# Optimization experiments

Hardware: AMD Instinct MI355X
Metric: run time of the kernel (lower is better)

Reference implementation:

```python
import jax, jax.numpy as jnp
import numpy as np

B, S, H = 32768, 16, 16  # batch, seq_len, G_hiddensize (code requires H == S and H == latent_dim == 16)
LATENT = 16
DISC_DIMS = [(1, 32), (32, 16), (16, 8), (8, 16), (16, 32)]


def setup_inputs() -> dict:
    key = jax.random.key(0)
    ks = iter(jax.random.split(key, 64))
    def p(shape, scale=0.1):
        return (jax.random.normal(next(ks), shape, dtype=jnp.float32) * scale)
    inp = dict(
        values=jax.random.normal(next(ks), (B, S), dtype=jnp.float32),
        masks=jax.random.randint(next(ks), (B, S), 0, 2).astype(jnp.int32),
        g_fwd_Wih=p((4 * H, 1)), g_fwd_Whh=p((4 * H, H)), g_fwd_b=p((4 * H,)),
        g_bwd_Wih=p((4 * H, 1)), g_bwd_Whh=p((4 * H, H)), g_bwd_b=p((4 * H,)),
        imp_W=p((1, H)), imp_b=p((1,)),
        fc_W=p((LATENT, H)), fc_b=p((LATENT,)),
        dec_Wih=p((4 * H, LATENT)), dec_Whh=p((4 * H, H)), dec_b=p((4 * H,)),
        dec_out_W=p((1, H)), dec_out_b=p((1,)),
        disc_out_W=p((1, 32)), disc_out_b=p((1,)),
    )
    for k, (i, h) in enumerate(DISC_DIMS):
        inp[f"d_W_{k}"] = p((4 * h, i))
        inp[f"d_b_{k}"] = p((4 * h,))
    return inp


def lstm_cell(x, h, c, Wih, Whh, b):
    gates = x @ Wih.T + h @ Whh.T + b
    i, f, g, o = jnp.split(gates, 4, axis=-1)
    c = jax.nn.sigmoid(f) * c + jax.nn.sigmoid(i) * jnp.tanh(g)
    h = jax.nn.sigmoid(o) * jnp.tanh(c)
    return h, c


def _forward(values, masks, g_fwd_Wih, g_fwd_Whh, g_fwd_b, g_bwd_Wih, g_bwd_Whh, g_bwd_b,
             imp_W, imp_b, fc_W, fc_b, dec_Wih, dec_Whh, dec_b, dec_out_W, dec_out_b,
             disc_out_W, disc_out_b,
             d_W_0, d_b_0, d_W_1, d_b_1, d_W_2, d_b_2, d_W_3, d_b_3, d_W_4, d_b_4):
    dt = values.dtype
    Bsz = values.shape[0]
    x = values[:, :, None]                     # (B, S, 1)
    m = masks.astype(dt)[:, :, None]           # (B, S, 1)
    # NOTE: torch.flip along axis 2 (size 1) is a no-op, so the bwd cell sees the
    # same (un-reversed) sequence as the fwd cell -- faithfully reproduced here.
    zH = jnp.zeros((Bsz, H), dt)
    h_f, c_f = lstm_cell(jnp.full((Bsz, 1), 128.0, dt), zH, zH, g_fwd_Wih, g_fwd_Whh, g_fwd_b)
    h_b, c_b = lstm_cell(jnp.full((Bsz, 1), -128.0, dt), zH, zH, g_bwd_Wih, g_bwd_Whh, g_bwd_b)

    def gen_step(carry, xm):
        h_f, c_f, h_b, c_b = carry
        x_t, m_t = xm                          # (B,1) each
        cc_f = (1 - m_t) * x_t + m_t * (h_f @ imp_W.T + imp_b)
        cc_b = (1 - m_t) * x_t + m_t * (h_b @ imp_W.T + imp_b)
        h_f, c_f = lstm_cell(cc_f, h_f, c_f, g_fwd_Wih, g_fwd_Whh, g_fwd_b)
        h_b, c_b = lstm_cell(cc_b, h_b, c_b, g_bwd_Wih, g_bwd_Whh, g_bwd_b)
        return (h_f, c_f, h_b, c_b), None

    (h_f, c_f, h_b, c_b), _ = jax.lax.scan(
        gen_step, (h_f, c_f, h_b, c_b),
        (jnp.transpose(x, (1, 0, 2)), jnp.transpose(m, (1, 0, 2))))
    h = h_f + h_b                               # (B, H), H == S
    imputations = h.reshape(Bsz, S, 1)
    imputed = imputations * (1 - m) + x * m      # (B, S, 1)

    # Discriminator: torch calls each LSTMCell WITHOUT state every timestep, so
    # hidden/cell start at zero each call -> purely feedforward per (batch, t).
    # W_hh @ 0 == 0, so only W_ih and the combined bias matter. Vectorize over B*S.
    inp = imputed.reshape(Bsz * S, 1)
    for W, b in ((d_W_0, d_b_0), (d_W_1, d_b_1), (d_W_2, d_b_2), (d_W_3, d_b_3), (d_W_4, d_b_4)):
        gates = inp @ W.T + b
        i, f, g, o = jnp.split(gates, 4, axis=-1)
        cc = jax.nn.sigmoid(i) * jnp.tanh(g)
        inp = jax.nn.sigmoid(o) * jnp.tanh(cc)
    disc_output = (inp @ disc_out_W.T + disc_out_b).reshape(Bsz, S, 1)

    latent = h @ fc_W.T + fc_b                  # (B, 16)

    # Decoder: ignores latent values (only uses batch size); start token = 128s.
    hd = cd = jnp.zeros((Bsz, H), dt)
    hd, cd = lstm_cell(jnp.full((Bsz, LATENT), 128.0, dt), hd, cd, dec_Wih, dec_Whh, dec_b)

    def dec_step(carry, _):
        hd, cd = carry
        hd, cd = lstm_cell(cd, hd, cd, dec_Wih, dec_Whh, dec_b)
        return (hd, cd), hd @ dec_out_W.T + dec_out_b

    _, outs = jax.lax.scan(dec_step, (hd, cd), None, length=S)  # (S, B, 1)
    reconstructed = jnp.transpose(outs, (1, 0, 2))
    return imputed, disc_output, latent, reconstructed


def reference(values, masks, g_fwd_Wih, g_fwd_Whh, g_fwd_b, g_bwd_Wih, g_bwd_Whh, g_bwd_b,
              imp_W, imp_b, fc_W, fc_b, dec_Wih, dec_Whh, dec_b, dec_out_W, dec_out_b,
              disc_out_W, disc_out_b,
              d_W_0, d_b_0, d_W_1, d_b_1, d_W_2, d_b_2, d_W_3, d_b_3, d_W_4, d_b_4):
    return _forward(values, masks, g_fwd_Wih, g_fwd_Whh, g_fwd_b, g_bwd_Wih, g_bwd_Whh, g_bwd_b,
                    imp_W, imp_b, fc_W, fc_b, dec_Wih, dec_Whh, dec_b, dec_out_W, dec_out_b,
                    disc_out_W, disc_out_b,
                    d_W_0, d_b_0, d_W_1, d_b_1, d_W_2, d_b_2, d_W_3, d_b_3, d_W_4, d_b_4)
```

## Files before the change

### kernel.cpp

```cpp
#include <hip/hip_runtime.h>

#define BB 32768
#define BS (BB*16)

typedef __attribute__((ext_vector_type(8))) short bf8v;
typedef __attribute__((ext_vector_type(4))) float f4v;

#define RECO 64
#define TAB  128
#define NTAB 2049
#define HFO  8448
#define HBO  (HFO+BS)

#define PW0 0
#define PB0 96
#define PW1 192
#define PB1 1920
#define PW2 1968
#define PB2 2448
#define PW3 2472
#define PB3 3048
#define PW4 3096
#define PB4 5016
#define POW 5112
#define POB 5144
#define PNU 5148

#define WVF 848
#define SMF 3392

#define NSCAN 1024
#define NTABB 129
#define DECB  (NSCAN + NTABB)

__device__ __forceinline__ float sigm(float x){
    return __builtin_amdgcn_rcpf(1.f + __expf(-x));
}
__device__ __forceinline__ float tanh_f(float x){
    return 1.f - 2.f * __builtin_amdgcn_rcpf(1.f + __expf(2.f * x));
}
__device__ __forceinline__ float dunit(float gi, float gg, float go){
    return sigm(go) * tanh_f(sigm(gi) * tanh_f(gg));
}
__device__ __forceinline__ unsigned short f2bf(float f){
    union { float f; unsigned int i; } v; v.f = f;
    unsigned int x = v.i;
    unsigned int r = x + 0x7fffu + ((x >> 16) & 1u);
    return (unsigned short)(r >> 16);
}
__device__ __forceinline__ float bfu(unsigned short s){
    union { unsigned u; float f; } v; v.u = ((unsigned)s) << 16; return v.f;
}
__device__ __forceinline__ float bflo(unsigned p){
    union { unsigned u; float f; } v; v.u = p << 16; return v.f;
}
__device__ __forceinline__ float bfhi(unsigned p){
    union { unsigned u; float f; } v; v.u = p & 0xffff0000u; return v.f;
}

struct P29 { const float* p[29]; };

__device__ __forceinline__ bf8v makeB(const float* Whh, const float* Wih,
                                      int row, int quad)
{
    bf8v B = {0,0,0,0,0,0,0,0};
    if (quad < 2) {
        const float4* p = (const float4*)(Whh + row*16 + quad*8);
        float4 a0 = p[0], a1 = p[1];
        B[0]=(short)f2bf(a0.x); B[1]=(short)f2bf(a0.y);
        B[2]=(short)f2bf(a0.z); B[3]=(short)f2bf(a0.w);
        B[4]=(short)f2bf(a1.x); B[5]=(short)f2bf(a1.y);
        B[6]=(short)f2bf(a1.z); B[7]=(short)f2bf(a1.w);
    } else if (quad == 2) {
        B[0] = (short)f2bf(Wih[row]);
    }
    return B;
}

__global__ __launch_bounds__(256)
void k_main(P29 a, const int* __restrict__ masks, float* __restrict__ ws)
{
    __shared__ __align__(16) float smem[SMF];
    int tid = threadIdx.x;

    if (blockIdx.x < NSCAN) {
        int lane = tid & 63;
        int wv   = tid >> 6;
        int n    = lane & 15;
        int quad = lane >> 4;
        int dir  = (int)(blockIdx.x >= 512);
        int gid0 = blockIdx.x * 64 + wv * 16;
        int b0   = gid0 & 32767;
        float* wbase = smem + wv * WVF;
        float* xs    = wbase;
        int*   msI   = (int*)(wbase + 320);
        unsigned short* hbp = (unsigned short*)(wbase + 640);
        float* ccf   = wbase + 832;
        const int4* hbI = (const int4*)hbp;
        {
            size_t gbase = (size_t)b0 * 16;
            int e = lane * 4;
            float4 xv = *(const float4*)(a.p[0] + gbase + e);
            int4   mv = *(const int4*)(masks + gbase + e);
            int sm = lane >> 2;
            int st = (lane & 3) * 4;
            xs[(st+0)*20 + sm] = xv.x;  msI[(st+0)*20 + sm] = mv.x;
            xs[(st+1)*20 + sm] = xv.y;  msI[(st+1)*20 + sm] = mv.y;
            xs[(st+2)*20 + sm] = xv.z;  msI[(st+2)*20 + sm] = mv.z;
            xs[(st+3)*20 + sm] = xv.w;  msI[(st+3)*20 + sm] = mv.w;
        }
        const float* __restrict__ Wih = a.p[2 + 3*dir];
        const float* __restrict__ Whh = a.p[3 + 3*dir];
        const float* __restrict__ bia = a.p[4 + 3*dir];
        bf8v Bi = makeB(Whh, Wih, n,      quad);
        bf8v Bf = makeB(Whh, Wih, 16+n,   quad);
        bf8v Bg = makeB(Whh, Wih, 32+n,   quad);
        bf8v Bo = makeB(Whh, Wih, 48+n,   quad);
        bf8v Bp = {0,0,0,0,0,0,0,0};
        if (quad < 2) {
            const float4* p = (const float4*)(a.p[8] + quad*8);
            float4 a0 = p[0], a1 = p[1];
            Bp[0]=(short)f2bf(a0.x); Bp[1]=(short)f2bf(a0.y);
            Bp[2]=(short)f2bf(a0.z); Bp[3]=(short)f2bf(a0.w);
            Bp[4]=(short)f2bf(a1.x); Bp[5]=(short)f2bf(a1.y);
            Bp[6]=(short)f2bf(a1.z); Bp[7]=(short)f2bf(a1.w);
        }
        float impb = a.p[9][0];
        float bi_ = bia[n], bf_ = bia[16+n], bg_ = bia[32+n], bo_ = bia[48+n];
        float sgn = dir ? -128.f : 128.f;
        float c0, h0;
        {
            float gi0 = sgn*Wih[n]    + bi_;
            float gg0 = sgn*Wih[32+n] + bg_;
            float go0 = sgn*Wih[48+n] + bo_;
            c0 = sigm(gi0) * tanh_f(gg0);
            h0 = sigm(go0) * tanh_f(c0);
        }
        float c[4] = {c0, c0, c0, c0};
        float h[4];
        {
            unsigned short hb0 = f2bf(h0);
            #pragma unroll
            for (int r = 0; r < 4; r++) hbp[(quad*4+r)*24 + n] = hb0;
        }
        const f4v cz = {0.f, 0.f, 0.f, 0.f};
        const bf8v Az = {0,0,0,0,0,0,0,0};
        for (int t = 0; t < 16; t++) {
            union { int4 i4; bf8v b; } au;
            au.i4 = hbI[n*3 + (quad & 1)];
            bf8v A = (quad < 2) ? au.b : Az;
            f4v dimp = __builtin_amdgcn_mfma_f32_16x16x32_bf16(A, Bp, cz, 0, 0, 0);
            float4 xt4 = *(const float4*)(xs + t*20 + quad*4);
            int4   mt4 = *(const int4*)(msI + t*20 + quad*4);
            float cc0 = mt4.x ? (dimp[0] + impb) : xt4.x;
            float cc1 = mt4.y ? (dimp[1] + impb) : xt4.y;
            float cc2 = mt4.z ? (dimp[2] + impb) : xt4.z;
            float cc3 = mt4.w ? (dimp[3] + impb) : xt4.w;
            if (n == 0) {
                ccf[quad*4+0] = cc0; ccf[quad*4+1] = cc1;
                ccf[quad*4+2] = cc2; ccf[quad*4+3] = cc3;
            }
            if (quad == 2) A[0] = (short)f2bf(ccf[n]);
            f4v di = __builtin_amdgcn_mfma_f32_16x16x32_bf16(A, Bi, cz, 0, 0, 0);
            f4v df = __builtin_amdgcn_mfma_f32_16x16x32_bf16(A, Bf, cz, 0, 0, 0);
            f4v dg = __builtin_amdgcn_mfma_f32_16x16x32_bf16(A, Bg, cz, 0, 0, 0);
            f4v dO = __builtin_amdgcn_mfma_f32_16x16x32_bf16(A, Bo, cz, 0, 0, 0);
            #pragma unroll
            for (int r = 0; r < 4; r++) {
                float gi = di[r] + bi_;
                float gf = df[r] + bf_;
                float gg = dg[r] + bg_;
                float go = dO[r] + bo_;
                float cn = sigm(gf)*c[r] + sigm(gi)*tanh_f(gg);
                c[r] = cn;
                float hh = sigm(go)*tanh_f(cn);
                h[r] = hh;
                hbp[(quad*4+r)*24 + n] = f2bf(hh);
            }
        }
        float* outp = ws + HFO + (size_t)dir*BS + (size_t)b0*16;
        #pragma unroll
        for (int r = 0; r < 4; r++) outp[(quad*4+r)*16 + n] = h[r];
        return;
    }

    if (blockIdx.x < DECB) {
        unsigned short* wl = (unsigned short*)smem;
#define STAGE(WS, BSi, h, K, padK, wdst, bdst) \
    { const float* Wp = a.p[WS]; const float* Bp2 = a.p[BSi]; \
      for (int i = tid; i < 3*(h)*(K); i += 256){ \
        int r = i/(K), k = i - r*(K); int g = r/(h), u0 = r - g*(h); \
        int sr = (g==0? u0 : (g==1? 2*(h)+u0 : 3*(h)+u0)); \
        wl[(wdst) + r*(padK) + k] = f2bf(Wp[sr*(K) + k]); } \
      for (int i = tid; i < 3*(h); i += 256){ \
        int g = i/(h), u0 = i - g*(h); \
        int sr = (g==0? u0 : (g==1? 2*(h)+u0 : 3*(h)+u0)); \
        wl[(bdst) + i] = f2bf(Bp2[sr]); } }
        STAGE(19, 20, 32,  1,  1, PW0, PB0)
        STAGE(21, 22, 16, 32, 36, PW1, PB1)
        STAGE(23, 24,  8, 16, 20, PW2, PB2)
        STAGE(25, 26, 16,  8, 12, PW3, PB3)
        STAGE(27, 28, 32, 16, 20, PW4, PB4)
#undef STAGE
        { const float* s = a.p[17]; for (int i = tid; i < 32; i += 256) wl[POW+i] = f2bf(s[i]); }
        if (tid == 0) wl[POB] = f2bf(a.p[18][0]);
        __syncthreads();
        int u = tid & 15;
        int gbase = (tid & 63) & 48;
        int gid = (blockIdx.x - NSCAN) * 16 + (tid >> 4);
        const uint2* w2 = (const uint2*)wl;
        float xin = -8.f + (float)gid * (1.f/128.f);
        float lo = dunit(xin*bfu(wl[PW0+u])    + bfu(wl[PB0+u]),
                         xin*bfu(wl[PW0+32+u]) + bfu(wl[PB0+32+u]),
                         xin*bfu(wl[PW0+64+u]) + bfu(wl[PB0+64+u]));
        float hi = dunit(xin*bfu(wl[PW0+16+u]) + bfu(wl[PB0+16+u]),
                         xin*bfu(wl[PW0+48+u]) + bfu(wl[PB0+48+u]),
                         xin*bfu(wl[PW0+80+u]) + bfu(wl[PB0+80+u]));
        float A0[32];
        #pragma unroll
        for (int k = 0; k < 16; k++) { A0[k] = __shfl(lo, gbase+k); A0[16+k] = __shfl(hi, gbase+k); }
        float gi = bfu(wl[PB1+u]), gg = bfu(wl[PB1+16+u]), go = bfu(wl[PB1+32+u]);
        int bi_ = (PW1 + u*36)>>2, bg_ = (PW1 + (16+u)*36)>>2, bo_ = (PW1 + (32+u)*36)>>2;
        #pragma unroll
        for (int q = 0; q < 8; q++) {
            uint2 wi = w2[bi_+q], wg = w2[bg_+q], wo = w2[bo_+q];
            float b0=A0[4*q], b1=A0[4*q+1], b2=A0[4*q+2], b3=A0[4*q+3];
            gi += b0*bflo(wi.x) + b1*bfhi(wi.x) + b2*bflo(wi.y) + b3*bfhi(wi.y);
            gg += b0*bflo(wg.x) + b1*bfhi(wg.x) + b2*bflo(wg.y) + b3*bfhi(wg.y);
            go += b0*bflo(wo.x) + b1*bfhi(wo.x) + b2*bflo(wo.y) + b3*bfhi(wo.y);
        }
        float a1 = dunit(gi, gg, go);
        float A1[16];
        #pragma unroll
        for (int k = 0; k < 16; k++) A1[k] = __shfl(a1, gbase+k);
        int v = u & 7;
        gi = bfu(wl[PB2+v]); gg = bfu(wl[PB2+8+v]); go = bfu(wl[PB2+16+v]);
        bi_ = (PW2 + v*20)>>2; bg_ = (PW2 + (8+v)*20)>>2; bo_ = (PW2 + (16+v)*20)>>2;
        #pragma unroll
        for (int q = 0; q < 4; q++) {
            uint2 wi = w2[bi_+q], wg = w2[bg_+q], wo = w2[bo_+q];
            float b0=A1[4*q], b1=A1[4*q+1], b2=A1[4*q+2], b3=A1[4*q+3];
            gi += b0*bflo(wi.x) + b1*bfhi(wi.x) + b2*bflo(wi.y) + b3*bfhi(wi.y);
            gg += b0*bflo(wg.x) + b1*bfhi(wg.x) + b2*bflo(wg.y) + b3*bfhi(wg.y);
            go += b0*bflo(wo.x) + b1*bfhi(wo.x) + b2*bflo(wo.y) + b3*bfhi(wo.y);
        }
        float a2 = dunit(gi, gg, go);
        float A2[8];
        #pragma unroll
        for (int k = 0; k < 8; k++) A2[k] = __shfl(a2, gbase+k);
        gi = bfu(wl[PB3+u]); gg = bfu(wl[PB3+16+u]); go = bfu(wl[PB3+32+u]);
        bi_ = (PW3 + u*12)>>2; bg_ = (PW3 + (16+u)*12)>>2; bo_ = (PW3 + (32+u)*12)>>2;
        #pragma unroll
        for (int q = 0; q < 2; q++) {
            uint2 wi = w2[bi_+q], wg = w2[bg_+q], wo = w2[bo_+q];
            float b0=A2[4*q], b1=A2[4*q+1], b2=A2[4*q+2], b3=A2[4*q+3];
            gi += b0*bflo(wi.x) + b1*bfhi(wi.x) + b2*bflo(wi.y) + b3*bfhi(wi.y);
            gg += b0*bflo(wg.x) + b1*bfhi(wg.x) + b2*bflo(wg.y) + b3*bfhi(wg.y);
            go += b0*bflo(wo.x) + b1*bfhi(wo.x) + b2*bflo(wo.y) + b3*bfhi(wo.y);
        }
        float a3 = dunit(gi, gg, go);
        float A3[16];
        #pragma unroll
        for (int k = 0; k < 16; k++) A3[k] = __shfl(a3, gbase+k);
        float part;
        {
            float g0i = bfu(wl[PB4+u]),    g0g = bfu(wl[PB4+32+u]), g0o = bfu(wl[PB4+64+u]);
            float g1i = bfu(wl[PB4+16+u]), g1g = bfu(wl[PB4+48+u]), g1o = bfu(wl[PB4+80+u]);
            int c0i = (PW4 + u*20)>>2,      c0g = (PW4 + (32+u)*20)>>2, c0o = (PW4 + (64+u)*20)>>2;
            int c1i = (PW4 + (16+u)*20)>>2, c1g = (PW4 + (48+u)*20)>>2, c1o = (PW4 + (80+u)*20)>>2;
            #pragma unroll
            for (int q = 0; q < 4; q++) {
                float b0=A3[4*q], b1=A3[4*q+1], b2=A3[4*q+2], b3=A3[4*q+3];
                uint2 wi = w2[c0i+q], wg = w2[c0g+q], wo = w2[c0o+q];
                g0i += b0*bflo(wi.x) + b1*bfhi(wi.x) + b2*bflo(wi.y) + b3*bfhi(wi.y);
                g0g += b0*bflo(wg.x) + b1*bfhi(wg.x) + b2*bflo(wg.y) + b3*bfhi(wg.y);
                g0o += b0*bflo(wo.x) + b1*bfhi(wo.x) + b2*bflo(wo.y) + b3*bfhi(wo.y);
                wi = w2[c1i+q]; wg = w2[c1g+q]; wo = w2[c1o+q];
                g1i += b0*bflo(wi.x) + b1*bfhi(wi.x) + b2*bflo(wi.y) + b3*bfhi(wi.y);
                g1g += b0*bflo(wg.x) + b1*bfhi(wg.x) + b2*bflo(wg.y) + b3*bfhi(wg.y);
                g1o += b0*bflo(wo.x) + b1*bfhi(wo.x) + b2*bflo(wo.y) + b3*bfhi(wo.y);
            }
            part = dunit(g0i, g0g, g0o)*bfu(wl[POW+u]) + dunit(g1i, g1g, g1o)*bfu(wl[POW+16+u]);
        }
        part += __shfl_xor(part, 1);
        part += __shfl_xor(part, 2);
        part += __shfl_xor(part, 4);
        part += __shfl_xor(part, 8);
        if (u == 0 && gid < NTAB) ws[TAB + gid] = part + bfu(wl[POB]);
        return;
    }

    {
        float* dh = smem;
        float* dc = smem + 16;
        const float* Wih = a.p[12];
        const float* Whh = a.p[13];
        const float* bb  = a.p[14];
        const float* oW  = a.p[15];
        const float* ob  = a.p[16];
        float wii[16], wff[16], wgg[16], woo[16];
        float vii[16], vff[16], vgg[16], voo[16];
        float bi_r=0, bf_r=0, bg_r=0, bo_r=0;
        if (tid < 16) {
            int uu = tid;
            #pragma unroll
            for (int k = 0; k < 16; k++) {
                wii[k]=Wih[uu*16+k];      vii[k]=Whh[uu*16+k];
                wff[k]=Wih[(16+uu)*16+k]; vff[k]=Whh[(16+uu)*16+k];
                wgg[k]=Wih[(32+uu)*16+k]; vgg[k]=Whh[(32+uu)*16+k];
                woo[k]=Wih[(48+uu)*16+k]; voo[k]=Whh[(48+uu)*16+k];
            }
            bi_r=bb[uu]; bf_r=bb[16+uu]; bg_r=bb[32+uu]; bo_r=bb[48+uu];
            float gi = bi_r, gg = bg_r, go = bo_r;
            #pragma unroll
            for (int k = 0; k < 16; k++) {
                gi += 128.f * wii[k];
                gg += 128.f * wgg[k];
                go += 128.f * woo[k];
            }
            float cd0 = sigm(gi) * tanh_f(gg);
            dc[tid] = cd0; dh[tid] = sigm(go) * tanh_f(cd0);
        }
        __syncthreads();
        for (int t = 0; t < 16; t++) {
            float rx[16], rh[16], cold = 0.f;
            if (tid < 16) {
                #pragma unroll
                for (int k = 0; k < 16; k++) { rx[k] = dc[k]; rh[k] = dh[k]; }
                cold = dc[tid];
            }
            __syncthreads();
            if (tid < 16) {
                float gi = bi_r, gf = bf_r, gg = bg_r, go = bo_r;
                #pragma unroll
                for (int k = 0; k < 16; k++) {
                    gi += rx[k]*wii[k] + rh[k]*vii[k];
                    gf += rx[k]*wff[k] + rh[k]*vff[k];
                    gg += rx[k]*wgg[k] + rh[k]*vgg[k];
                    go += rx[k]*woo[k] + rh[k]*voo[k];
                }
                float cn = sigm(gf)*cold + sigm(gi)*tanh_f(gg);
                dc[tid] = cn; dh[tid] = sigm(go)*tanh_f(cn);
            }
            __syncthreads();
            if (tid == 0) {
                float o = ob[0];
                #pragma unroll
                for (int k = 0; k < 16; k++) o += dh[k] * oW[k];
                ws[RECO + t] = o;
            }
            __syncthreads();
        }
    }
}

__global__ __launch_bounds__(256) void k_post(P29 a, const int* __restrict__ masks,
                                              const float* __restrict__ ws,
                                              float* __restrict__ out)
{
    __shared__ float tab[NTAB];
    __shared__ __align__(16) float fw[256];
    __shared__ __align__(16) float rec[16];
    __shared__ float fb[16];
    int tid = threadIdx.x;
    for (int i = tid; i < NTAB; i += 256) tab[i] = ws[TAB + i];
    fw[tid] = a.p[10][tid];
    if (tid < 16) { fb[tid] = a.p[11][tid]; rec[tid] = ws[RECO + tid]; }
    __syncthreads();
    int T = blockIdx.x * 256 + tid;
    int b = T >> 2;
    int q = T & 3;
    int tq = q * 4;
    const float4* hf4 = (const float4*)(ws + HFO + (size_t)b*16);
    const float4* hb4 = (const float4*)(ws + HBO + (size_t)b*16);
    float4 s0, s1, s2, s3;
    {
        float4 f0=hf4[0], f1=hf4[1], f2=hf4[2], f3=hf4[3];
        float4 g0=hb4[0], g1=hb4[1], g2=hb4[2], g3=hb4[3];
        s0 = make_float4(f0.x+g0.x, f0.y+g0.y, f0.z+g0.z, f0.w+g0.w);
        s1 = make_float4(f1.x+g1.x, f1.y+g1.y, f1.z+g1.z, f1.w+g1.w);
        s2 = make_float4(f2.x+g2.x, f2.y+g2.y, f2.z+g2.z, f2.w+g2.w);
        s3 = make_float4(f3.x+g3.x, f3.y+g3.y, f3.z+g3.z, f3.w+g3.w);
    }
    float4 hq = (q==0) ? s0 : (q==1) ? s1 : (q==2) ? s2 : s3;
    float4 xv = *(const float4*)(a.p[0] + (size_t)b*16 + tq);
    int4   mv = *(const int4*)(masks + (size_t)b*16 + tq);
    float impv[4];
    impv[0] = mv.x ? xv.x : hq.x;
    impv[1] = mv.y ? xv.y : hq.y;
    impv[2] = mv.z ? xv.z : hq.z;
    impv[3] = mv.w ? xv.w : hq.w;
    float latv[4];
    #pragma unroll
    for (int j = 0; j < 4; j++) {
        int t = tq + j;
        const float4* wr = (const float4*)(fw + t*16);
        float4 w0=wr[0], w1=wr[1], w2=wr[2], w3=wr[3];
        float l = fb[t];
        l += s0.x*w0.x + s0.y*w0.y + s0.z*w0.z + s0.w*w0.w;
        l += s1.x*w1.x + s1.y*w1.y + s1.z*w1.z + s1.w*w1.w;
        l += s2.x*w2.x + s2.y*w2.y + s2.z*w2.z + s2.w*w2.w;
        l += s3.x*w3.x + s3.y*w3.y + s3.z*w3.z + s3.w*w3.w;
        latv[j] = l;
    }
    float dv[4];
    #pragma unroll
    for (int j = 0; j < 4; j++) {
        float xx = fminf(fmaxf(impv[j], -8.f), 8.f);
        float f = (xx + 8.f) * 128.f;
        float fi = floorf(f);
        int i = (int)fi; i = i > NTAB-2 ? NTAB-2 : i;
        float w = f - fi;
        dv[j] = fmaf(w, tab[i+1] - tab[i], tab[i]);
    }
    float4 rv = ((const float4*)rec)[q];
    size_t eo = (size_t)b*16 + tq;
    *(float4*)(out + eo)        = make_float4(impv[0], impv[1], impv[2], impv[3]);
    *(float4*)(out + BS + eo)   = make_float4(dv[0], dv[1], dv[2], dv[3]);
    *(float4*)(out + 2*BS + eo) = make_float4(latv[0], latv[1], latv[2], latv[3]);
    *(float4*)(out + 3*BS + eo) = rv;
}

extern "C" void kernel_launch(void* const* d_in, const int* in_sizes, int n_in,
                              void* d_out, int out_size, void* d_ws, size_t ws_size,
                              hipStream_t stream)
{
    float* ws = (float*)d_ws;
    P29 a;
    for (int i = 0; i < 29; i++) a.p[i] = (const float*)d_in[i];
    const int* masks = (const int*)d_in[1];
    k_main<<<NSCAN + NTABB + 1, 256, 0, stream>>>(a, masks, ws);
    k_post<<<(BB*4)/256, 256, 0, stream>>>(a, masks, ws, (float*)d_out);
}
```

Baseline: 164.2 us.

## Transpose scan MFMA operands, pass hidden state via bpermute, reorder block roles

The generator LSTM scan now treats the weights as the MFMA A operand and the hidden state as B, so each lane holds one batch row. The recurrent state moves between lanes with ds_bpermute and packed bf16 converts instead of round-tripping through shared memory. Biases are folded into the MFMA accumulator inputs, and x and mask values are read straight from global per row instead of being staged in LDS. Block order also changes so the decoder and table blocks run first, and the shared memory footprint shrinks, which may raise occupancy. In exchange the per-step lane exchange adds bpermute latency on the serial dependency chain, and the output store pattern changes.

After: 154.0 us. 1.07x faster.

```diff
diff --git a/kernel.cpp b/kernel.cpp
--- a/kernel.cpp
+++ b/kernel.cpp
@@ -26,12 +26,10 @@
 #define POB 5144
 #define PNU 5148
 
-#define WVF 848
-#define SMF 3392
+#define SMF 2580
 
 #define NSCAN 1024
 #define NTABB 129
-#define DECB  (NSCAN + NTABB)
 
 __device__ __forceinline__ float sigm(float x){
     return __builtin_amdgcn_rcpf(1.f + __expf(-x));
@@ -83,108 +81,118 @@
     __shared__ __align__(16) float smem[SMF];
     int tid = threadIdx.x;
 
-    if (blockIdx.x < NSCAN) {
+    if (blockIdx.x >= NTABB + 1) {
         int lane = tid & 63;
         int wv   = tid >> 6;
-        int n    = lane & 15;
+        int m    = lane & 15;
         int quad = lane >> 4;
-        int dir  = (int)(blockIdx.x >= 512);
-        int gid0 = blockIdx.x * 64 + wv * 16;
+        int sb   = blockIdx.x - (NTABB + 1);
+        int dir  = sb >= 512 ? 1 : 0;
+        int gid0 = sb * 64 + wv * 16;
         int b0   = gid0 & 32767;
-        float* wbase = smem + wv * WVF;
-        float* xs    = wbase;
-        int*   msI   = (int*)(wbase + 320);
-        unsigned short* hbp = (unsigned short*)(wbase + 640);
-        float* ccf   = wbase + 832;
-        const int4* hbI = (const int4*)hbp;
-        {
-            size_t gbase = (size_t)b0 * 16;
-            int e = lane * 4;
-            float4 xv = *(const float4*)(a.p[0] + gbase + e);
-            int4   mv = *(const int4*)(masks + gbase + e);
-            int sm = lane >> 2;
-            int st = (lane & 3) * 4;
-            xs[(st+0)*20 + sm] = xv.x;  msI[(st+0)*20 + sm] = mv.x;
-            xs[(st+1)*20 + sm] = xv.y;  msI[(st+1)*20 + sm] = mv.y;
-            xs[(st+2)*20 + sm] = xv.z;  msI[(st+2)*20 + sm] = mv.z;
-            xs[(st+3)*20 + sm] = xv.w;  msI[(st+3)*20 + sm] = mv.w;
-        }
+
         const float* __restrict__ Wih = a.p[2 + 3*dir];
         const float* __restrict__ Whh = a.p[3 + 3*dir];
         const float* __restrict__ bia = a.p[4 + 3*dir];
-        bf8v Bi = makeB(Whh, Wih, n,      quad);
-        bf8v Bf = makeB(Whh, Wih, 16+n,   quad);
-        bf8v Bg = makeB(Whh, Wih, 32+n,   quad);
-        bf8v Bo = makeB(Whh, Wih, 48+n,   quad);
-        bf8v Bp = {0,0,0,0,0,0,0,0};
+
+        bf8v Ai = makeB(Whh, Wih, m,      quad);
+        bf8v Af = makeB(Whh, Wih, 16+m,   quad);
+        bf8v Ag = makeB(Whh, Wih, 32+m,   quad);
+        bf8v Ao = makeB(Whh, Wih, 48+m,   quad);
+        bf8v Ap = {0,0,0,0,0,0,0,0};
         if (quad < 2) {
             const float4* p = (const float4*)(a.p[8] + quad*8);
             float4 a0 = p[0], a1 = p[1];
-            Bp[0]=(short)f2bf(a0.x); Bp[1]=(short)f2bf(a0.y);
-            Bp[2]=(short)f2bf(a0.z); Bp[3]=(short)f2bf(a0.w);
-            Bp[4]=(short)f2bf(a1.x); Bp[5]=(short)f2bf(a1.y);
-            Bp[6]=(short)f2bf(a1.z); Bp[7]=(short)f2bf(a1.w);
+            Ap[0]=(short)f2bf(a0.x); Ap[1]=(short)f2bf(a0.y);
+            Ap[2]=(short)f2bf(a0.z); Ap[3]=(short)f2bf(a0.w);
+            Ap[4]=(short)f2bf(a1.x); Ap[5]=(short)f2bf(a1.y);
+            Ap[6]=(short)f2bf(a1.z); Ap[7]=(short)f2bf(a1.w);
         }
         float impb = a.p[9][0];
-        float bi_ = bia[n], bf_ = bia[16+n], bg_ = bia[32+n], bo_ = bia[48+n];
+        f4v cimp = {impb, impb, impb, impb};
+
+        f4v cbi, cbf, cbg, cbo;
+        {
+            float4 t;
+            t = *(const float4*)(bia +      quad*4); cbi = (f4v){t.x,t.y,t.z,t.w};
+            t = *(const float4*)(bia + 16 + quad*4); cbf = (f4v){t.x,t.y,t.z,t.w};
+            t = *(const float4*)(bia + 32 + quad*4); cbg = (f4v){t.x,t.y,t.z,t.w};
+            t = *(const float4*)(bia + 48 + quad*4); cbo = (f4v){t.x,t.y,t.z,t.w};
+        }
+
         float sgn = dir ? -128.f : 128.f;
-        float c0, h0;
+        float c[4], hl[4];
         {
-            float gi0 = sgn*Wih[n]    + bi_;
-            float gg0 = sgn*Wih[32+n] + bg_;
-            float go0 = sgn*Wih[48+n] + bo_;
-            c0 = sigm(gi0) * tanh_f(gg0);
-            h0 = sigm(go0) * tanh_f(c0);
-        }
-        float c[4] = {c0, c0, c0, c0};
-        float h[4];
-        {
-            unsigned short hb0 = f2bf(h0);
-            #pragma unroll
-            for (int r = 0; r < 4; r++) hbp[(quad*4+r)*24 + n] = hb0;
-        }
-        const f4v cz = {0.f, 0.f, 0.f, 0.f};
-        const bf8v Az = {0,0,0,0,0,0,0,0};
-        for (int t = 0; t < 16; t++) {
-            union { int4 i4; bf8v b; } au;
-            au.i4 = hbI[n*3 + (quad & 1)];
-            bf8v A = (quad < 2) ? au.b : Az;
-            f4v dimp = __builtin_amdgcn_mfma_f32_16x16x32_bf16(A, Bp, cz, 0, 0, 0);
-            float4 xt4 = *(const float4*)(xs + t*20 + quad*4);
-            int4   mt4 = *(const int4*)(msI + t*20 + quad*4);
-            float cc0 = mt4.x ? (dimp[0] + impb) : xt4.x;
-            float cc1 = mt4.y ? (dimp[1] + impb) : xt4.y;
-            float cc2 = mt4.z ? (dimp[2] + impb) : xt4.z;
-            float cc3 = mt4.w ? (dimp[3] + impb) : xt4.w;
-            if (n == 0) {
-                ccf[quad*4+0] = cc0; ccf[quad*4+1] = cc1;
-                ccf[quad*4+2] = cc2; ccf[quad*4+3] = cc3;
-            }
-            if (quad == 2) A[0] = (short)f2bf(ccf[n]);
-            f4v di = __builtin_amdgcn_mfma_f32_16x16x32_bf16(A, Bi, cz, 0, 0, 0);
-            f4v df = __builtin_amdgcn_mfma_f32_16x16x32_bf16(A, Bf, cz, 0, 0, 0);
-            f4v dg = __builtin_amdgcn_mfma_f32_16x16x32_bf16(A, Bg, cz, 0, 0, 0);
-            f4v dO = __builtin_amdgcn_mfma_f32_16x16x32_bf16(A, Bo, cz, 0, 0, 0);
+            float4 wI = *(const float4*)(Wih +      quad*4);
+            float4 wG = *(const float4*)(Wih + 32 + quad*4);
+            float4 wO = *(const float4*)(Wih + 48 + quad*4);
+            float wIv[4] = {wI.x, wI.y, wI.z, wI.w};
+            float wGv[4] = {wG.x, wG.y, wG.z, wG.w};
+            float wOv[4] = {wO.x, wO.y, wO.z, wO.w};
             #pragma unroll
             for (int r = 0; r < 4; r++) {
-                float gi = di[r] + bi_;
-                float gf = df[r] + bf_;
-                float gg = dg[r] + bg_;
-                float go = dO[r] + bo_;
-                float cn = sigm(gf)*c[r] + sigm(gi)*tanh_f(gg);
-                c[r] = cn;
-                float hh = sigm(go)*tanh_f(cn);
-                h[r] = hh;
-                hbp[(quad*4+r)*24 + n] = f2bf(hh);
+                float gi0 = sgn*wIv[r] + cbi[r];
+                float gg0 = sgn*wGv[r] + cbg[r];
+                float go0 = sgn*wOv[r] + cbo[r];
+                float c0 = sigm(gi0) * tanh_f(gg0);
+                c[r] = c0;
+                hl[r] = sigm(go0) * tanh_f(c0);
+            }
+        }
+        unsigned u01, u23;
+        asm("v_cvt_pk_bf16_f32 %0, %1, %2" : "=v"(u01) : "v"(hl[0]), "v"(hl[1]));
+        asm("v_cvt_pk_bf16_f32 %0, %1, %2" : "=v"(u23) : "v"(hl[2]), "v"(hl[3]));
+
+        int pa0 = ((m + quad*32)      & 63) << 2;
+        int pa1 = ((m + quad*32 + 16) & 63) << 2;
+
+        const float* xrow = a.p[0] + (size_t)(b0 + m) * 16;
+        const int*   mrow = masks  + (size_t)(b0 + m) * 16;
+
+        #pragma unroll
+        for (int t4 = 0; t4 < 4; t4++) {
+            float4 x4 = *(const float4*)(xrow + t4*4);
+            int4   m4 = *(const int4*)(mrow + t4*4);
+            float xa[4] = {x4.x, x4.y, x4.z, x4.w};
+            int   ma[4] = {m4.x, m4.y, m4.z, m4.w};
+            #pragma unroll
+            for (int j = 0; j < 4; j++) {
+                union { int i[4]; bf8v v; } B;
+                int w0 = __builtin_amdgcn_ds_bpermute(pa0, (int)u01);
+                int w1 = __builtin_amdgcn_ds_bpermute(pa0, (int)u23);
+                int w2 = __builtin_amdgcn_ds_bpermute(pa1, (int)u01);
+                int w3 = __builtin_amdgcn_ds_bpermute(pa1, (int)u23);
+                bool hi2 = quad >= 2;
+                B.i[0] = hi2 ? 0 : w0;
+                B.i[1] = hi2 ? 0 : w1;
+                B.i[2] = hi2 ? 0 : w2;
+                B.i[3] = hi2 ? 0 : w3;
+                f4v dimp = __builtin_amdgcn_mfma_f32_16x16x32_bf16(Ap, B.v, cimp, 0, 0, 0);
+                float cc = ma[j] ? dimp[0] : xa[j];
+                unsigned ccw;
+                asm("v_cvt_pk_bf16_f32 %0, %1, %2" : "=v"(ccw) : "v"(cc), "v"(0.f));
+                B.i[0] = (quad == 2) ? (int)ccw : B.i[0];
+                f4v di  = __builtin_amdgcn_mfma_f32_16x16x32_bf16(Ai, B.v, cbi, 0, 0, 0);
+                f4v df_ = __builtin_amdgcn_mfma_f32_16x16x32_bf16(Af, B.v, cbf, 0, 0, 0);
+                f4v dg  = __builtin_amdgcn_mfma_f32_16x16x32_bf16(Ag, B.v, cbg, 0, 0, 0);
+                f4v dO  = __builtin_amdgcn_mfma_f32_16x16x32_bf16(Ao, B.v, cbo, 0, 0, 0);
+                #pragma unroll
+                for (int r = 0; r < 4; r++) {
+                    float cn = sigm(df_[r]) * c[r] + sigm(di[r]) * tanh_f(dg[r]);
+                    c[r] = cn;
+                    hl[r] = sigm(dO[r]) * tanh_f(cn);
+                }
+                asm("v_cvt_pk_bf16_f32 %0, %1, %2" : "=v"(u01) : "v"(hl[0]), "v"(hl[1]));
+                asm("v_cvt_pk_bf16_f32 %0, %1, %2" : "=v"(u23) : "v"(hl[2]), "v"(hl[3]));
             }
         }
         float* outp = ws + HFO + (size_t)dir*BS + (size_t)b0*16;
         #pragma unroll
-        for (int r = 0; r < 4; r++) outp[(quad*4+r)*16 + n] = h[r];
+        for (int r = 0; r < 4; r++) outp[m*16 + quad*4 + r] = hl[r];
         return;
     }
 
-    if (blockIdx.x < DECB) {
+    if (blockIdx.x >= 1) {
         unsigned short* wl = (unsigned short*)smem;
 #define STAGE(WS, BSi, h, K, padK, wdst, bdst) \
     { const float* Wp = a.p[WS]; const float* Bp2 = a.p[BSi]; \
@@ -207,7 +215,7 @@
         __syncthreads();
         int u = tid & 15;
         int gbase = (tid & 63) & 48;
-        int gid = (blockIdx.x - NSCAN) * 16 + (tid >> 4);
+        int gid = (blockIdx.x - 1) * 16 + (tid >> 4);
         const uint2* w2 = (const uint2*)wl;
         float xin = -8.f + (float)gid * (1.f/128.f);
         float lo = dunit(xin*bfu(wl[PW0+u])    + bfu(wl[PB0+u]),
@@ -429,6 +437,6 @@
     P29 a;
     for (int i = 0; i < 29; i++) a.p[i] = (const float*)d_in[i];
     const int* masks = (const int*)d_in[1];
-    k_main<<<NSCAN + NTABB + 1, 256, 0, stream>>>(a, masks, ws);
+    k_main<<<1 + NTABB + NSCAN, 256, 0, stream>>>(a, masks, ws);
     k_post<<<(BB*4)/256, 256, 0, stream>>>(a, masks, ws, (float*)d_out);
 }
```
